# Performance work log

Hardware: AMD Instinct MI355X
Metric: run time of the kernel (lower is better)

Reference implementation:

```python
import jax, jax.numpy as jnp
import numpy as np

BATCH, IN_F, OUT_F = 4096, 1024, 1024


def setup_inputs() -> dict:
    key = jax.random.key(0)
    kx, kw = jax.random.split(key)
    x = jax.random.normal(kx, (BATCH, IN_F, 4), dtype=jnp.float32)
    weight = jax.random.normal(kw, (OUT_F, IN_F, 4), dtype=jnp.float32) * 0.01
    bias = jnp.zeros((OUT_F, 4), dtype=jnp.float32)
    return {"x": x, "weight": weight, "bias": bias}


def reference(x, weight, bias):
    # x: (batch, in, 4) quaternions; weight: (out, in, 4); bias: (out, 4)
    # Hamilton product broadcast over (batch, out, in) then summed over in ==
    # 16 signed real GEMMs contracting the `in` dimension.
    ar, ai, aj, ak = x[..., 0], x[..., 1], x[..., 2], x[..., 3]          # (b, i)
    br, bi, bj, bk = weight[..., 0], weight[..., 1], weight[..., 2], weight[..., 3]  # (o, i)

    mm = lambda a, w: jnp.einsum('bi,oi->bo', a, w)

    out_r = mm(ar, br) - mm(ai, bi) - mm(aj, bj) - mm(ak, bk)
    out_i = mm(ar, bi) + mm(ai, br) + mm(aj, bk) - mm(ak, bj)
    out_j = mm(ar, bj) - mm(ai, bk) + mm(aj, br) + mm(ak, bi)
    out_k = mm(ar, bk) + mm(ai, bj) - mm(aj, bi) + mm(ak, br)

    out = jnp.stack([out_r, out_i, out_j, out_k], axis=-1)  # (b, o, 4)
    return out + bias
```

## Files before the change

kernel.cpp:

```cpp
#include <hip/hip_runtime.h>


typedef __bf16 bf16x8 __attribute__((ext_vector_type(8)));
typedef float floatx4 __attribute__((ext_vector_type(4)));

constexpr int M = 4096;
constexpr int N = 4096;
constexpr int K = 4096;
constexpr int BM = 256, BN = 256, BK = 64;
constexpr int TILES = K / BK;

constexpr int CVT_BLOCKS = (M * K / 8) / 256;
constexpr int EXP_BLOCKS = (1024 * 1024 / 2) / 256;

#define BARRIER() asm volatile("s_barrier" ::: "memory")
#define LDS_OFF(p) ((unsigned)(uintptr_t)(__attribute__((address_space(3))) const void*)(p))

__global__ void prep_kernel(const float* __restrict__ x, const float* __restrict__ w,
                            __bf16* __restrict__ A, __bf16* __restrict__ Wb) {
    const int b = blockIdx.x;
    if (b < CVT_BLOCKS) {
        const size_t i = (size_t)b * 256 + threadIdx.x;
        const float4* xp = (const float4*)x;
        float4 a = xp[2 * i];
        float4 c = xp[2 * i + 1];
        bf16x8 v;
        v[0] = (__bf16)a.x; v[1] = (__bf16)a.y; v[2] = (__bf16)a.z; v[3] = (__bf16)a.w;
        v[4] = (__bf16)c.x; v[5] = (__bf16)c.y; v[6] = (__bf16)c.z; v[7] = (__bf16)c.w;
        *(bf16x8*)(A + 8 * i) = v;
    } else {
        const int idx = (b - CVT_BLOCKS) * 256 + threadIdx.x;
        const int o  = idx >> 9;
        const int ip = (idx & 511) * 2;
        float4 q0 = ((const float4*)w)[o * 1024 + ip];
        float4 q1 = ((const float4*)w)[o * 1024 + ip + 1];
        __bf16* base = Wb + (size_t)(o * 4) * K + ip * 4;
        bf16x8 r;
        r[0] = (__bf16)q0.x; r[1] = (__bf16)(-q0.y); r[2] = (__bf16)(-q0.z); r[3] = (__bf16)(-q0.w);
        r[4] = (__bf16)q1.x; r[5] = (__bf16)(-q1.y); r[6] = (__bf16)(-q1.z); r[7] = (__bf16)(-q1.w);
        *(bf16x8*)(base) = r;
        r[0] = (__bf16)q0.y; r[1] = (__bf16)q0.x; r[2] = (__bf16)q0.w; r[3] = (__bf16)(-q0.z);
        r[4] = (__bf16)q1.y; r[5] = (__bf16)q1.x; r[6] = (__bf16)q1.w; r[7] = (__bf16)(-q1.z);
        *(bf16x8*)(base + (size_t)K) = r;
        r[0] = (__bf16)q0.z; r[1] = (__bf16)(-q0.w); r[2] = (__bf16)q0.x; r[3] = (__bf16)q0.y;
        r[4] = (__bf16)q1.z; r[5] = (__bf16)(-q1.w); r[6] = (__bf16)q1.x; r[7] = (__bf16)q1.y;
        *(bf16x8*)(base + (size_t)2 * K) = r;
        r[0] = (__bf16)q0.w; r[1] = (__bf16)q0.z; r[2] = (__bf16)(-q0.y); r[3] = (__bf16)q0.x;
        r[4] = (__bf16)q1.w; r[5] = (__bf16)q1.z; r[6] = (__bf16)(-q1.y); r[7] = (__bf16)q1.x;
        *(bf16x8*)(base + (size_t)3 * K) = r;
    }
}

__device__ __forceinline__ void gload_lds16(const __bf16* g, __bf16* l) {
    __builtin_amdgcn_global_load_lds(
        (const __attribute__((address_space(1))) void*)g,
        (__attribute__((address_space(3))) void*)l, 16, 0, 0);
}

__device__ __forceinline__ bf16x8 dsr128(unsigned addr) {
    bf16x8 r;
    asm volatile("ds_read_b128 %0, %1" : "=v"(r) : "v"(addr));
    return r;
}

__global__ __launch_bounds__(512, 2) void qgemm_kernel(const __bf16* __restrict__ A,
                                                       const __bf16* __restrict__ B,
                                                       const float* __restrict__ bias,
                                                       float* __restrict__ C) {
    __shared__ __bf16 As[2][BM][BK];
    __shared__ __bf16 Bs[2][BN][BK];

    const int tid  = threadIdx.x;
    const int wave = tid >> 6;
    const int lane = tid & 63;

    const int bid = blockIdx.x;
    const int xcd = bid & 7;
    const int q   = bid >> 3;
    const int tm  = (xcd >> 2) * 8 + (q & 7);
    const int tn  = (xcd & 3) * 4 + (q >> 3);
    const int bm  = tm * BM;
    const int bn  = tn * BN;

    const int wm = (wave >> 2) * 128;
    const int wn = (wave & 3) * 64;

    const int srow = wave * 16 + (lane >> 3);
    const int schk = ((lane & 7) ^ (lane >> 3)) * 8;
    const __bf16* agA = A + (size_t)(bm + srow) * K + schk;
    const __bf16* agB = B + (size_t)(bn + srow) * K + schk;

    auto issueA = [&](int buf, int h, int t) {
        const __bf16* g = agA + (size_t)h * 128 * K + t * BK;
        gload_lds16(g,                 &As[buf][h * 128 + wave * 16][0]);
        gload_lds16(g + (size_t)8 * K, &As[buf][h * 128 + wave * 16 + 8][0]);
    };
    auto issueB = [&](int buf, int h, int t) {
        const __bf16* g = agB + (size_t)h * 128 * K + t * BK;
        gload_lds16(g,                 &Bs[buf][h * 128 + wave * 16][0]);
        gload_lds16(g + (size_t)8 * K, &Bs[buf][h * 128 + wave * 16 + 8][0]);
    };

    const int fl  = lane & 15;
    const int fq  = lane >> 4;
    const int fx7 = fl & 7;
    const unsigned ebo0 = (unsigned)(((fq)     ^ fx7) * 16);
    const unsigned ebo1 = (unsigned)(((4 + fq) ^ fx7) * 16);
    const unsigned aRow = LDS_OFF(&As[0][0][0]) + (unsigned)(wm + fl) * 128u;
    const unsigned bRow = LDS_OFF(&Bs[0][0][0]) + (unsigned)(wn + fl) * 128u;

    floatx4 acc[8][4] = {};
    bf16x8 bF[4][2];

    issueA(0, 0, 0); issueA(0, 1, 0);
    issueB(0, 0, 0); issueB(0, 1, 0);
    issueB(1, 0, 1); issueB(1, 1, 1);
    asm volatile("s_waitcnt vmcnt(4)");
    BARRIER();

    for (int t = 0; t < TILES; ++t) {
        const int b  = t & 1;
        const unsigned bs = (unsigned)b * 32768u;
#pragma unroll
        for (int p = 0; p < 4; ++p) {
            const unsigned pa = bs + (unsigned)(p * 4096);
            bf16x8 aL0 = dsr128(aRow + pa + ebo0);
            bf16x8 aL1 = dsr128(aRow + pa + ebo1);
            bf16x8 aH0 = dsr128(aRow + pa + 2048u + ebo0);
            bf16x8 aH1 = dsr128(aRow + pa + 2048u + ebo1);
            if (p == 0) {
#pragma unroll
                for (int nt = 0; nt < 4; ++nt) {
                    bF[nt][0] = dsr128(bRow + bs + (unsigned)(nt * 2048) + ebo0);
                    bF[nt][1] = dsr128(bRow + bs + (unsigned)(nt * 2048) + ebo1);
                }
            }
            if (p == 0 && t + 1 < TILES) { issueA(b ^ 1, 0, t + 1); issueA(b ^ 1, 1, t + 1); }
            if (p == 2 && t + 2 < TILES) issueB(b, 0, t + 2);
            if (p == 3 && t + 2 < TILES) issueB(b, 1, t + 2);
            BARRIER();
            asm volatile("s_waitcnt lgkmcnt(0)");
            __builtin_amdgcn_sched_barrier(0);
            __builtin_amdgcn_s_setprio(1);
#pragma unroll
            for (int nt = 0; nt < 4; ++nt) {
                acc[2 * p][nt]     = __builtin_amdgcn_mfma_f32_16x16x32_bf16(
                    aL0, bF[nt][0], acc[2 * p][nt], 0, 0, 0);
                acc[2 * p + 1][nt] = __builtin_amdgcn_mfma_f32_16x16x32_bf16(
                    aH0, bF[nt][0], acc[2 * p + 1][nt], 0, 0, 0);
            }
#pragma unroll
            for (int nt = 0; nt < 4; ++nt) {
                acc[2 * p][nt]     = __builtin_amdgcn_mfma_f32_16x16x32_bf16(
                    aL1, bF[nt][1], acc[2 * p][nt], 0, 0, 0);
                acc[2 * p + 1][nt] = __builtin_amdgcn_mfma_f32_16x16x32_bf16(
                    aH1, bF[nt][1], acc[2 * p + 1][nt], 0, 0, 0);
            }
            __builtin_amdgcn_s_setprio(0);
            if (p == 3) {
                if (t + 2 < TILES) asm volatile("s_waitcnt vmcnt(4)");
                else               asm volatile("s_waitcnt vmcnt(0)");
            }
            BARRIER();
        }
    }

#pragma unroll
    for (int mt = 0; mt < 8; ++mt) {
        const int row = bm + wm + mt * 16 + fq * 4;
#pragma unroll
        for (int nt = 0; nt < 4; ++nt) {
            const int col = bn + wn + nt * 16 + fl;
            const float bv = bias[col];
            float* cp = C + (size_t)row * N + col;
#pragma unroll
            for (int r = 0; r < 4; ++r)
                cp[(size_t)r * N] = acc[mt][nt][r] + bv;
        }
    }
}

extern "C" void kernel_launch(void* const* d_in, const int* in_sizes, int n_in,
                              void* d_out, int out_size, void* d_ws, size_t ws_size,
                              hipStream_t stream) {
    const float* x    = (const float*)d_in[0];
    const float* w    = (const float*)d_in[1];
    const float* bias = (const float*)d_in[2];
    float* out = (float*)d_out;

    __bf16* Abf  = (__bf16*)d_ws;
    __bf16* Wbig = (__bf16*)((char*)d_ws + (size_t)M * K * 2);

    prep_kernel<<<CVT_BLOCKS + EXP_BLOCKS, 256, 0, stream>>>(x, w, Abf, Wbig);

    qgemm_kernel<<<256, 512, 0, stream>>>(Abf, Wbig, bias, out);
}
```

Measured before the change: 251.0 us.

## Software-pipeline A-fragment LDS reads with MFMAs and cut barriers per tile

The per-tile loop used four phases, each with two block barriers and a full LDS wait before its MFMAs. It is replaced by a single synchronisation point per K tile. All B fragments and the first A fragments are read up front, and later A fragments are double-buffered in registers (x/y) so each group's ds_reads overlap the previous group's MFMAs. Both halves of the next-next B tile are now issued right after the first barrier. The aim is to cut barrier stalls and LDS latency exposure, at the cost of more live VGPRs and tighter ordering assumptions on buffer reuse.

```diff
diff --git a/kernel.cpp b/kernel.cpp
--- a/kernel.cpp
+++ b/kernel.cpp
@@ -14,6 +14,8 @@
 constexpr int EXP_BLOCKS = (1024 * 1024 / 2) / 256;
 
 #define BARRIER() asm volatile("s_barrier" ::: "memory")
+#define LGKM0()   do { asm volatile("s_waitcnt lgkmcnt(0)"); __builtin_amdgcn_sched_barrier(0); } while (0)
+#define SB()      __builtin_amdgcn_sched_barrier(0)
 #define LDS_OFF(p) ((unsigned)(uintptr_t)(__attribute__((address_space(3))) const void*)(p))
 
 __global__ void prep_kernel(const float* __restrict__ x, const float* __restrict__ w,
@@ -112,8 +114,28 @@
     floatx4 acc[8][4] = {};
     bf16x8 bF[4][2];
 
+#define MFMA_PAIR(i0, i1, a0, a1, a2, a3)                                        \
+    do {                                                                         \
+        __builtin_amdgcn_s_setprio(1);                                           \
+        _Pragma("unroll")                                                        \
+        for (int nt = 0; nt < 4; ++nt) {                                         \
+            acc[i0][nt] = __builtin_amdgcn_mfma_f32_16x16x32_bf16(               \
+                a0, bF[nt][0], acc[i0][nt], 0, 0, 0);                            \
+            acc[i1][nt] = __builtin_amdgcn_mfma_f32_16x16x32_bf16(               \
+                a2, bF[nt][0], acc[i1][nt], 0, 0, 0);                            \
+        }                                                                        \
+        _Pragma("unroll")                                                        \
+        for (int nt = 0; nt < 4; ++nt) {                                         \
+            acc[i0][nt] = __builtin_amdgcn_mfma_f32_16x16x32_bf16(               \
+                a1, bF[nt][1], acc[i0][nt], 0, 0, 0);                            \
+            acc[i1][nt] = __builtin_amdgcn_mfma_f32_16x16x32_bf16(               \
+                a3, bF[nt][1], acc[i1][nt], 0, 0, 0);                            \
+        }                                                                        \
+        __builtin_amdgcn_s_setprio(0);                                           \
+    } while (0)
+
+    issueB(0, 0, 0); issueB(0, 1, 0);
     issueA(0, 0, 0); issueA(0, 1, 0);
-    issueB(0, 0, 0); issueB(0, 1, 0);
     issueB(1, 0, 1); issueB(1, 1, 1);
     asm volatile("s_waitcnt vmcnt(4)");
     BARRIER();
@@ -121,48 +143,52 @@
     for (int t = 0; t < TILES; ++t) {
         const int b  = t & 1;
         const unsigned bs = (unsigned)b * 32768u;
-#pragma unroll
-        for (int p = 0; p < 4; ++p) {
-            const unsigned pa = bs + (unsigned)(p * 4096);
-            bf16x8 aL0 = dsr128(aRow + pa + ebo0);
-            bf16x8 aL1 = dsr128(aRow + pa + ebo1);
-            bf16x8 aH0 = dsr128(aRow + pa + 2048u + ebo0);
-            bf16x8 aH1 = dsr128(aRow + pa + 2048u + ebo1);
-            if (p == 0) {
-#pragma unroll
-                for (int nt = 0; nt < 4; ++nt) {
-                    bF[nt][0] = dsr128(bRow + bs + (unsigned)(nt * 2048) + ebo0);
-                    bF[nt][1] = dsr128(bRow + bs + (unsigned)(nt * 2048) + ebo1);
-                }
-            }
-            if (p == 0 && t + 1 < TILES) { issueA(b ^ 1, 0, t + 1); issueA(b ^ 1, 1, t + 1); }
-            if (p == 2 && t + 2 < TILES) issueB(b, 0, t + 2);
-            if (p == 3 && t + 2 < TILES) issueB(b, 1, t + 2);
-            BARRIER();
-            asm volatile("s_waitcnt lgkmcnt(0)");
-            __builtin_amdgcn_sched_barrier(0);
-            __builtin_amdgcn_s_setprio(1);
-#pragma unroll
-            for (int nt = 0; nt < 4; ++nt) {
-                acc[2 * p][nt]     = __builtin_amdgcn_mfma_f32_16x16x32_bf16(
-                    aL0, bF[nt][0], acc[2 * p][nt], 0, 0, 0);
-                acc[2 * p + 1][nt] = __builtin_amdgcn_mfma_f32_16x16x32_bf16(
-                    aH0, bF[nt][0], acc[2 * p + 1][nt], 0, 0, 0);
-            }
-#pragma unroll
-            for (int nt = 0; nt < 4; ++nt) {
-                acc[2 * p][nt]     = __builtin_amdgcn_mfma_f32_16x16x32_bf16(
-                    aL1, bF[nt][1], acc[2 * p][nt], 0, 0, 0);
-                acc[2 * p + 1][nt] = __builtin_amdgcn_mfma_f32_16x16x32_bf16(
-                    aH1, bF[nt][1], acc[2 * p + 1][nt], 0, 0, 0);
-            }
-            __builtin_amdgcn_s_setprio(0);
-            if (p == 3) {
-                if (t + 2 < TILES) asm volatile("s_waitcnt vmcnt(4)");
-                else               asm volatile("s_waitcnt vmcnt(0)");
-            }
-            BARRIER();
+        const unsigned aB = aRow + bs;
+
+#pragma unroll
+        for (int nt = 0; nt < 4; ++nt) {
+            bF[nt][0] = dsr128(bRow + bs + (unsigned)(nt * 2048) + ebo0);
+            bF[nt][1] = dsr128(bRow + bs + (unsigned)(nt * 2048) + ebo1);
         }
+        bf16x8 x0 = dsr128(aB + ebo0);
+        bf16x8 x1 = dsr128(aB + ebo1);
+        bf16x8 x2 = dsr128(aB + 2048u + ebo0);
+        bf16x8 x3 = dsr128(aB + 2048u + ebo1);
+        if (t + 1 < TILES) { issueA(b ^ 1, 0, t + 1); issueA(b ^ 1, 1, t + 1); }
+        LGKM0();
+        BARRIER();
+        if (t + 2 < TILES) { issueB(b, 0, t + 2); issueB(b, 1, t + 2); }
+        SB();
+
+        bf16x8 y0 = dsr128(aB + 4096u + ebo0);
+        bf16x8 y1 = dsr128(aB + 4096u + ebo1);
+        bf16x8 y2 = dsr128(aB + 4096u + 2048u + ebo0);
+        bf16x8 y3 = dsr128(aB + 4096u + 2048u + ebo1);
+        SB();
+        MFMA_PAIR(0, 1, x0, x1, x2, x3);
+        LGKM0();
+
+        x0 = dsr128(aB + 8192u + ebo0);
+        x1 = dsr128(aB + 8192u + ebo1);
+        x2 = dsr128(aB + 8192u + 2048u + ebo0);
+        x3 = dsr128(aB + 8192u + 2048u + ebo1);
+        SB();
+        MFMA_PAIR(2, 3, y0, y1, y2, y3);
+        LGKM0();
+
+        y0 = dsr128(aB + 12288u + ebo0);
+        y1 = dsr128(aB + 12288u + ebo1);
+        y2 = dsr128(aB + 12288u + 2048u + ebo0);
+        y3 = dsr128(aB + 12288u + 2048u + ebo1);
+        SB();
+        MFMA_PAIR(4, 5, x0, x1, x2, x3);
+        LGKM0();
+
+        MFMA_PAIR(6, 7, y0, y1, y2, y3);
+        SB();
+        if (t + 2 < TILES)      asm volatile("s_waitcnt vmcnt(4)");
+        else if (t + 1 < TILES) asm volatile("s_waitcnt vmcnt(0)");
+        BARRIER();
     }
 
 #pragma unroll
@@ -178,6 +204,7 @@
                 cp[(size_t)r * N] = acc[mt][nt][r] + bv;
         }
     }
+#undef MFMA_PAIR
 }
 
 extern "C" void kernel_launch(void* const* d_in, const int* in_sizes, int n_in,
```

Result: no change. 247.5 us (-1.4%).

## Software-pipeline LDS fragment reads across MFMA phases with two barriers per tile

Applied to the files above, without the earlier changes.

Rewrites the GEMM main loop as a manually unrolled two-tile macro pipeline. LDS reads for the next A/B fragments are issued before the MFMAs that consume the current fragments, with partial lgkmcnt waits in between. This cuts the block barriers from eight per K-tile to two and lets ds_read latency overlap matrix math. In exchange it needs more live fragment registers, and it relies on a full vmcnt(0) wait plus barrier placement to avoid buffer hazards, which may hurt occupancy or stall on global loads.

```diff
diff --git a/kernel.cpp b/kernel.cpp
--- a/kernel.cpp
+++ b/kernel.cpp
@@ -14,6 +14,9 @@
 constexpr int EXP_BLOCKS = (1024 * 1024 / 2) / 256;
 
 #define BARRIER() asm volatile("s_barrier" ::: "memory")
+#define SB()      __builtin_amdgcn_sched_barrier(0)
+#define LGKM0()   do { asm volatile("s_waitcnt lgkmcnt(0)"); SB(); } while (0)
+#define LGKM4()   do { asm volatile("s_waitcnt lgkmcnt(4)"); SB(); } while (0)
 #define LDS_OFF(p) ((unsigned)(uintptr_t)(__attribute__((address_space(3))) const void*)(p))
 
 __global__ void prep_kernel(const float* __restrict__ x, const float* __restrict__ w,
@@ -110,59 +113,150 @@
     const unsigned bRow = LDS_OFF(&Bs[0][0][0]) + (unsigned)(wn + fl) * 128u;
 
     floatx4 acc[8][4] = {};
-    bf16x8 bF[4][2];
-
+    bf16x8 x0, x1, x2, x3, y0, y1, y2, y3;
+    bf16x8 bE0, bE1, bE2, bE3, bO0, bO1, bO2, bO3;
+    bf16x8 s0, s1, s2, s3;
+
+#define HALF(i0, i1, AA, AB, F0, F1, F2, F3)                                      \
+    acc[i0][0] = __builtin_amdgcn_mfma_f32_16x16x32_bf16(AA, F0, acc[i0][0], 0, 0, 0); \
+    acc[i1][0] = __builtin_amdgcn_mfma_f32_16x16x32_bf16(AB, F0, acc[i1][0], 0, 0, 0); \
+    acc[i0][1] = __builtin_amdgcn_mfma_f32_16x16x32_bf16(AA, F1, acc[i0][1], 0, 0, 0); \
+    acc[i1][1] = __builtin_amdgcn_mfma_f32_16x16x32_bf16(AB, F1, acc[i1][1], 0, 0, 0); \
+    acc[i0][2] = __builtin_amdgcn_mfma_f32_16x16x32_bf16(AA, F2, acc[i0][2], 0, 0, 0); \
+    acc[i1][2] = __builtin_amdgcn_mfma_f32_16x16x32_bf16(AB, F2, acc[i1][2], 0, 0, 0); \
+    acc[i0][3] = __builtin_amdgcn_mfma_f32_16x16x32_bf16(AA, F3, acc[i0][3], 0, 0, 0); \
+    acc[i1][3] = __builtin_amdgcn_mfma_f32_16x16x32_bf16(AB, F3, acc[i1][3], 0, 0, 0)
+
+#define TILE(T, BUFC, BC0, BC1, BC2, BC3, BX0, BX1, BX2, BX3, ISSB)               \
+    do {                                                                          \
+        const unsigned bsc_ = (BUFC) * 32768u;                                    \
+        const unsigned bsn_ = (1 - (BUFC)) * 32768u;                              \
+                \
+        issueA(1 - (BUFC), 0, (T) + 1); issueA(1 - (BUFC), 1, (T) + 1);           \
+        s0 = dsr128(bRow + bsc_ + 0u    + ebo1);                                  \
+        s1 = dsr128(bRow + bsc_ + 2048u + ebo1);                                  \
+        s2 = dsr128(bRow + bsc_ + 4096u + ebo1);                                  \
+        s3 = dsr128(bRow + bsc_ + 6144u + ebo1);                                  \
+        y0 = dsr128(aRow + bsc_ + 4096u + ebo0);                                  \
+        y1 = dsr128(aRow + bsc_ + 4096u + ebo1);                                  \
+        y2 = dsr128(aRow + bsc_ + 6144u + ebo0);                                  \
+        y3 = dsr128(aRow + bsc_ + 6144u + ebo1);                                  \
+        SB();                                                                     \
+        __builtin_amdgcn_s_setprio(1);                                            \
+        HALF(0, 1, x0, x2, BC0, BC1, BC2, BC3);                                   \
+        __builtin_amdgcn_s_setprio(0);                                            \
+        LGKM4();                                    \
+        __builtin_amdgcn_s_setprio(1);                                            \
+        HALF(0, 1, x1, x3, s0, s1, s2, s3);                                       \
+        __builtin_amdgcn_s_setprio(0);                                            \
+        LGKM0();                                                                  \
+              \
+        x0 = dsr128(aRow + bsc_ + 8192u  + ebo0);                                 \
+        x1 = dsr128(aRow + bsc_ + 8192u  + ebo1);                                 \
+        x2 = dsr128(aRow + bsc_ + 10240u + ebo0);                                 \
+        x3 = dsr128(aRow + bsc_ + 10240u + ebo1);                                 \
+        SB();                                                                     \
+        __builtin_amdgcn_s_setprio(1);                                            \
+        HALF(2, 3, y0, y2, BC0, BC1, BC2, BC3);                                   \
+        HALF(2, 3, y1, y3, s0, s1, s2, s3);                                       \
+        __builtin_amdgcn_s_setprio(0);                                            \
+        LGKM0();                                                                  \
+        asm volatile("s_waitcnt vmcnt(0)");       \
+        BARRIER();                                        \
+        if (ISSB) { issueB((BUFC), 0, (T) + 2); issueB((BUFC), 1, (T) + 2); }     \
+                 \
+        y0 = dsr128(aRow + bsc_ + 12288u + ebo0);                                 \
+        y1 = dsr128(aRow + bsc_ + 12288u + ebo1);                                 \
+        y2 = dsr128(aRow + bsc_ + 14336u + ebo0);                                 \
+        y3 = dsr128(aRow + bsc_ + 14336u + ebo1);                                 \
+        BX0 = dsr128(bRow + bsn_ + 0u    + ebo0);                                 \
+        BX1 = dsr128(bRow + bsn_ + 2048u + ebo0);                                 \
+        BX2 = dsr128(bRow + bsn_ + 4096u + ebo0);                                 \
+        BX3 = dsr128(bRow + bsn_ + 6144u + ebo0);                                 \
+        SB();                                                                     \
+        __builtin_amdgcn_s_setprio(1);                                            \
+        HALF(4, 5, x0, x2, BC0, BC1, BC2, BC3);                                   \
+        HALF(4, 5, x1, x3, s0, s1, s2, s3);                                       \
+        __builtin_amdgcn_s_setprio(0);                                            \
+        LGKM4();                                   \
+                            \
+        x0 = dsr128(aRow + bsn_ + 0u    + ebo0);                                  \
+        x1 = dsr128(aRow + bsn_ + 0u    + ebo1);                                  \
+        x2 = dsr128(aRow + bsn_ + 2048u + ebo0);                                  \
+        x3 = dsr128(aRow + bsn_ + 2048u + ebo1);                                  \
+        SB();                                                                     \
+        __builtin_amdgcn_s_setprio(1);                                            \
+        HALF(6, 7, y0, y2, BC0, BC1, BC2, BC3);                                   \
+        HALF(6, 7, y1, y3, s0, s1, s2, s3);                                       \
+        __builtin_amdgcn_s_setprio(0);                                            \
+        LGKM0();                                         \
+        BARRIER();                               \
+    } while (0)
+
+    issueB(0, 0, 0); issueB(0, 1, 0);
     issueA(0, 0, 0); issueA(0, 1, 0);
-    issueB(0, 0, 0); issueB(0, 1, 0);
     issueB(1, 0, 1); issueB(1, 1, 1);
     asm volatile("s_waitcnt vmcnt(4)");
     BARRIER();
-
-    for (int t = 0; t < TILES; ++t) {
-        const int b  = t & 1;
-        const unsigned bs = (unsigned)b * 32768u;
-#pragma unroll
-        for (int p = 0; p < 4; ++p) {
-            const unsigned pa = bs + (unsigned)(p * 4096);
-            bf16x8 aL0 = dsr128(aRow + pa + ebo0);
-            bf16x8 aL1 = dsr128(aRow + pa + ebo1);
-            bf16x8 aH0 = dsr128(aRow + pa + 2048u + ebo0);
-            bf16x8 aH1 = dsr128(aRow + pa + 2048u + ebo1);
-            if (p == 0) {
-#pragma unroll
-                for (int nt = 0; nt < 4; ++nt) {
-                    bF[nt][0] = dsr128(bRow + bs + (unsigned)(nt * 2048) + ebo0);
-                    bF[nt][1] = dsr128(bRow + bs + (unsigned)(nt * 2048) + ebo1);
-                }
-            }
-            if (p == 0 && t + 1 < TILES) { issueA(b ^ 1, 0, t + 1); issueA(b ^ 1, 1, t + 1); }
-            if (p == 2 && t + 2 < TILES) issueB(b, 0, t + 2);
-            if (p == 3 && t + 2 < TILES) issueB(b, 1, t + 2);
-            BARRIER();
-            asm volatile("s_waitcnt lgkmcnt(0)");
-            __builtin_amdgcn_sched_barrier(0);
-            __builtin_amdgcn_s_setprio(1);
-#pragma unroll
-            for (int nt = 0; nt < 4; ++nt) {
-                acc[2 * p][nt]     = __builtin_amdgcn_mfma_f32_16x16x32_bf16(
-                    aL0, bF[nt][0], acc[2 * p][nt], 0, 0, 0);
-                acc[2 * p + 1][nt] = __builtin_amdgcn_mfma_f32_16x16x32_bf16(
-                    aH0, bF[nt][0], acc[2 * p + 1][nt], 0, 0, 0);
-            }
-#pragma unroll
-            for (int nt = 0; nt < 4; ++nt) {
-                acc[2 * p][nt]     = __builtin_amdgcn_mfma_f32_16x16x32_bf16(
-                    aL1, bF[nt][1], acc[2 * p][nt], 0, 0, 0);
-                acc[2 * p + 1][nt] = __builtin_amdgcn_mfma_f32_16x16x32_bf16(
-                    aH1, bF[nt][1], acc[2 * p + 1][nt], 0, 0, 0);
-            }
-            __builtin_amdgcn_s_setprio(0);
-            if (p == 3) {
-                if (t + 2 < TILES) asm volatile("s_waitcnt vmcnt(4)");
-                else               asm volatile("s_waitcnt vmcnt(0)");
-            }
-            BARRIER();
-        }
+    bE0 = dsr128(bRow + 0u    + ebo0);
+    bE1 = dsr128(bRow + 2048u + ebo0);
+    bE2 = dsr128(bRow + 4096u + ebo0);
+    bE3 = dsr128(bRow + 6144u + ebo0);
+    x0  = dsr128(aRow + 0u    + ebo0);
+    x1  = dsr128(aRow + 0u    + ebo1);
+    x2  = dsr128(aRow + 2048u + ebo0);
+    x3  = dsr128(aRow + 2048u + ebo1);
+    LGKM0();
+
+    for (int t = 0; t < 62; t += 2) {
+        TILE(t,     0, bE0, bE1, bE2, bE3, bO0, bO1, bO2, bO3, true);
+        TILE(t + 1, 1, bO0, bO1, bO2, bO3, bE0, bE1, bE2, bE3, true);
+    }
+    TILE(62, 0, bE0, bE1, bE2, bE3, bO0, bO1, bO2, bO3, false);
+
+    {
+        const unsigned bsc_ = 32768u;
+        s0 = dsr128(bRow + bsc_ + 0u    + ebo1);
+        s1 = dsr128(bRow + bsc_ + 2048u + ebo1);
+        s2 = dsr128(bRow + bsc_ + 4096u + ebo1);
+        s3 = dsr128(bRow + bsc_ + 6144u + ebo1);
+        y0 = dsr128(aRow + bsc_ + 4096u + ebo0);
+        y1 = dsr128(aRow + bsc_ + 4096u + ebo1);
+        y2 = dsr128(aRow + bsc_ + 6144u + ebo0);
+        y3 = dsr128(aRow + bsc_ + 6144u + ebo1);
+        SB();
+        __builtin_amdgcn_s_setprio(1);
+        HALF(0, 1, x0, x2, bO0, bO1, bO2, bO3);
+        __builtin_amdgcn_s_setprio(0);
+        LGKM4();
+        __builtin_amdgcn_s_setprio(1);
+        HALF(0, 1, x1, x3, s0, s1, s2, s3);
+        __builtin_amdgcn_s_setprio(0);
+        LGKM0();
+        x0 = dsr128(aRow + bsc_ + 8192u  + ebo0);
+        x1 = dsr128(aRow + bsc_ + 8192u  + ebo1);
+        x2 = dsr128(aRow + bsc_ + 10240u + ebo0);
+        x3 = dsr128(aRow + bsc_ + 10240u + ebo1);
+        SB();
+        __builtin_amdgcn_s_setprio(1);
+        HALF(2, 3, y0, y2, bO0, bO1, bO2, bO3);
+        HALF(2, 3, y1, y3, s0, s1, s2, s3);
+        __builtin_amdgcn_s_setprio(0);
+        LGKM0();
+        y0 = dsr128(aRow + bsc_ + 12288u + ebo0);
+        y1 = dsr128(aRow + bsc_ + 12288u + ebo1);
+        y2 = dsr128(aRow + bsc_ + 14336u + ebo0);
+        y3 = dsr128(aRow + bsc_ + 14336u + ebo1);
+        SB();
+        __builtin_amdgcn_s_setprio(1);
+        HALF(4, 5, x0, x2, bO0, bO1, bO2, bO3);
+        HALF(4, 5, x1, x3, s0, s1, s2, s3);
+        __builtin_amdgcn_s_setprio(0);
+        LGKM0();
+        __builtin_amdgcn_s_setprio(1);
+        HALF(6, 7, y0, y2, bO0, bO1, bO2, bO3);
+        HALF(6, 7, y1, y3, s0, s1, s2, s3);
+        __builtin_amdgcn_s_setprio(0);
     }
 
 #pragma unroll
@@ -178,6 +272,8 @@
                 cp[(size_t)r * N] = acc[mt][nt][r] + bv;
         }
     }
+#undef TILE
+#undef HALF
 }
 
 extern "C" void kernel_launch(void* const* d_in, const int* in_sizes, int n_in,
```

After: 286.5 us. 1.14x slower.
